# Kernel tuning notes

Hardware: AMD Instinct MI355X
Metric: run time of the kernel (lower is better)

The kernel has to match this reference:

```python
import jax, jax.numpy as jnp
import numpy as np

B, S, UC = 64, 5, 50          # batch, sample (candidates), clicked history
D, T = 128, 768               # embedding_size, title_size
NE, NR, NN = 200000, 100, 50000  # entities, relations, news
K, A = 10, 20                 # neighbors per entity, anchor nodes per news


def _lin(k, out_d, in_d):
    w = jax.random.normal(k, (out_d, in_d), jnp.float32) * (1.0 / np.sqrt(in_d))
    b = jnp.zeros((out_d,), jnp.float32)
    return w, b


def setup_inputs() -> dict:
    key = jax.random.key(0)
    ks = jax.random.split(key, 16)
    W_nc1, b_nc1 = _lin(ks[0], D, T)
    W_nc2, b_nc2 = _lin(ks[1], D, D)
    W_anchor, b_anchor = _lin(ks[2], D, 2 * D)
    W_aw1, b_aw1 = _lin(ks[3], D, D)
    W_aw2, b_aw2 = _lin(ks[4], 1, D)
    W_mlp1, b_mlp1 = _lin(ks[5], D, 2 * D)
    W_mlp2, b_mlp2 = _lin(ks[6], D, D)
    return {
        "news_title_embedding": jax.random.normal(ks[7], (NN, T), jnp.float32),
        "entity_embedding": jax.random.normal(ks[8], (NE, D), jnp.float32),
        "relation_embedding": jax.random.normal(ks[9], (NR, D), jnp.float32),
        "W_nc1": W_nc1, "b_nc1": b_nc1, "W_nc2": W_nc2, "b_nc2": b_nc2,
        "W_anchor": W_anchor, "b_anchor": b_anchor,
        "W_aw1": W_aw1, "b_aw1": b_aw1, "W_aw2": W_aw2, "b_aw2": b_aw2,
        "W_mlp1": W_mlp1, "b_mlp1": b_mlp1, "W_mlp2": W_mlp2, "b_mlp2": b_mlp2,
        "cand_news": jax.random.randint(ks[10], (B, S), 0, NN, jnp.int32),
        "clicked_news": jax.random.randint(ks[11], (B, UC), 0, NN, jnp.int32),
        "cand_anchor_nodes": jax.random.randint(ks[12], (B * S, A), 0, NE, jnp.int32),
        "clicked_anchor_nodes": jax.random.randint(ks[13], (B * UC, A), 0, NE, jnp.int32),
        "entity_adj": jax.random.randint(ks[14], (NE, K), 0, NE, jnp.int32),
        "relation_adj": jax.random.randint(ks[15], (NE, K), 0, NR, jnp.int32),
    }


def reference(news_title_embedding, entity_embedding, relation_embedding,
              W_nc1, b_nc1, W_nc2, b_nc2,
              W_anchor, b_anchor, W_aw1, b_aw1, W_aw2, b_aw2,
              W_mlp1, b_mlp1, W_mlp2, b_mlp2,
              cand_news, clicked_news, cand_anchor_nodes, clicked_anchor_nodes,
              entity_adj, relation_adj):
    elu = jax.nn.elu

    def news_emb(ids_flat):  # [N] -> [N, D]
        t = news_title_embedding[ids_flat]                       # [N, T]
        return jnp.tanh(elu(t @ W_nc1.T + b_nc1) @ W_nc2.T + b_nc2)

    def anchor_graph_emb(nodes):  # [N, A] -> [N, D]
        node_e = entity_embedding[nodes]                          # [N, A, D]
        nb_ent = entity_embedding[entity_adj[nodes]]              # [N, A, K, D]
        nb_rel = relation_embedding[relation_adj[nodes]]          # [N, A, K, D]
        agg = jnp.sum(nb_ent + nb_rel, axis=-2)                   # [N, A, D]
        h = jnp.tanh(jnp.concatenate([node_e, agg], axis=-1) @ W_anchor.T + b_anchor)
        logits = elu(h @ W_aw1.T + b_aw1) @ W_aw2.T + b_aw2       # [N, A, 1]
        w = jax.nn.softmax(logits, axis=-2)                       # softmax over anchor nodes
        return jnp.sum(h * w, axis=-2)                            # [N, D]

    cand_e = news_emb(cand_news.reshape(-1))                      # [B*S, D]
    clk_e = news_emb(clicked_news.reshape(-1))                    # [B*UC, D]
    cand_e = jnp.concatenate([cand_e, anchor_graph_emb(cand_anchor_nodes)], axis=-1)
    clk_e = jnp.concatenate([clk_e, anchor_graph_emb(clicked_anchor_nodes)], axis=-1)

    def mlp(x):
        return elu(elu(x @ W_mlp1.T + b_mlp1) @ W_mlp2.T + b_mlp2)

    news_embedding = mlp(cand_e).reshape(B, S, -1)                # [B, S, D]
    user_embedding = jnp.mean(mlp(clk_e).reshape(B, UC, -1), axis=1)  # [B, D]
    score = jnp.sum(news_embedding * user_embedding[:, None, :], axis=-1)  # [B, S]
    return score
```

## Files before the change

### kernel.cpp

```cpp
#include <hip/hip_runtime.h>
#include <hip/hip_bf16.h>


#define B_ 64
#define S_ 5
#define UC_ 50
#define A_ 20
#define NCAND 320
#define NCLK 3200
#define NNEWS 3520
#define NANCH 70400

static constexpr long OFF_WNC1P = 64;
static constexpr long OFF_BNC1  = 98368;
static constexpr long OFF_WNC2P = 98496;
static constexpr long OFF_BNC2  = 114880;
static constexpr long OFF_WANCP = 115008;
static constexpr long OFF_BANC  = 147776;
static constexpr long OFF_WAW1P = 147904;
static constexpr long OFF_BAW1  = 164288;
static constexpr long OFF_WAW2  = 164416;
static constexpr long OFF_BAW2  = 164544;
static constexpr long OFF_WM1P  = 164548;
static constexpr long OFF_BM1   = 197316;
static constexpr long OFF_WM2P  = 197444;
static constexpr long OFF_BM2   = 213828;
static constexpr long OFF_REL   = 213956;
static constexpr long OFF_AE    = 226756;
static constexpr long OFF_NE    = 677316;
static constexpr long OFF_MO    = 1127876;
static constexpr long OFF_X     = 1578436;

typedef __attribute__((ext_vector_type(8))) short short8v;
typedef __attribute__((ext_vector_type(16))) float f32x16;

__device__ __forceinline__ float ldf(const void* p, long i, int bf) {
  if (bf) {
    unsigned int u = (unsigned int)((const unsigned short*)p)[i];
    u <<= 16;
    return __uint_as_float(u);
  }
  return ((const float*)p)[i];
}

__device__ __forceinline__ float4 ldf4(const void* p, long i, int bf) {
  float4 f;
  if (bf) {
    const unsigned short* q = (const unsigned short*)p + i;
    uint2 u = *(const uint2*)q;
    f.x = __uint_as_float(u.x << 16);
    f.y = __uint_as_float(u.x & 0xffff0000u);
    f.z = __uint_as_float(u.y << 16);
    f.w = __uint_as_float(u.y & 0xffff0000u);
  } else {
    f = *(const float4*)((const float*)p + i);
  }
  return f;
}

__device__ __forceinline__ float eluf(float v) { return v > 0.f ? v : expm1f(v); }

__device__ __forceinline__ void splitbf(float v, unsigned short& hi, unsigned short& lo) {
  unsigned int b = __float_as_uint(v);
  hi = (unsigned short)(b >> 16);
  float rm = v - __uint_as_float(b & 0xffff0000u);
  unsigned int rb = __float_as_uint(rm);
  lo = (unsigned short)((rb + 0x7fffu + ((rb >> 16) & 1u)) >> 16);
}

__device__ __forceinline__ float bfh(unsigned short u) {
  return __uint_as_float((unsigned int)u << 16);
}

__global__ void k_detect(const void* ent, int* flag) {
  __shared__ int cnt;
  if (threadIdx.x == 0) cnt = 0;
  __syncthreads();
  unsigned short u = ((const unsigned short*)ent)[threadIdx.x];
  int e = (u >> 7) & 0xFF;
  int ok = (e >= 107 && e <= 146) ? 1 : 0;
  atomicAdd(&cnt, ok);
  __syncthreads();
  if (threadIdx.x == 0) *flag = (cnt >= 200) ? 1 : 0;
}

__global__ __launch_bounds__(256) void k_prep(
    const void* s0, const void* s1, const void* s2, const void* s3,
    const void* s4, const void* s5, const void* s6, const void* s7,
    const void* s8, const void* s9, const void* s10, const void* s11,
    const void* s12, const void* s13, const void* s14, float* ws) {
  const int bf = ((const int*)ws)[0];
  const void* srcs[15] = {s0,s1,s2,s3,s4,s5,s6,s7,s8,s9,s10,s11,s12,s13,s14};
  const int R[15] = {128,128,128,128,128,128,128,128,1,  1,  128,128,128,128,100};
  const int C[15] = {768,1,  128,1,  256,1,  128,1,  128,1,  256,1,  128,1,  128};
  const int MD[15]= {2,  0,  2,  0,  3,  0,  3,  0,  0,  0,  2,  0,  2,  0,  0};
  const long OFF[15] = {OFF_WNC1P,OFF_BNC1,OFF_WNC2P,OFF_BNC2,OFF_WANCP,OFF_BANC,
                        OFF_WAW1P,OFF_BAW1,OFF_WAW2,OFF_BAW2,OFF_WM1P,OFF_BM1,
                        OFF_WM2P,OFF_BM2,OFF_REL};
  const long total = 226689;
  for (long idx = (long)blockIdx.x * blockDim.x + threadIdx.x; idx < total;
       idx += (long)gridDim.x * blockDim.x) {
    long rem = idx;
    int s = 0;
    while (rem >= (long)R[s] * C[s]) { rem -= (long)R[s] * C[s]; s++; }
    float v = ldf(srcs[s], rem, bf);
    if (MD[s] == 2) {
      long r = rem / C[s], c = rem - r * C[s];
      ws[OFF[s] + (c >> 2) * 512 + r * 4 + (c & 3)] = v;
    } else if (MD[s] == 3) {
      long r = rem / C[s], c = rem - r * C[s];
      unsigned short hi, lo;
      splitbf(v, hi, lo);
      unsigned short* H = (unsigned short*)(ws + OFF[s]);
      unsigned short* L = H + (s == 4 ? 32768 : 16384);
      long id2 = ((c >> 4) * 128 + r) * 16 + (c & 15);
      H[id2] = hi;
      L[id2] = lo;
    } else {
      ws[OFF[s] + rem] = v;
    }
  }
}

__global__ __launch_bounds__(128) void k_news(const void* titles, const int* cand,
                                              const int* clk, float* ws) {
  const int bf = ((const int*)ws)[0];
  __shared__ __align__(16) float t[8][768];
  __shared__ __align__(16) float h1[8][128];
  int tid = threadIdx.x;
  long r0 = (long)blockIdx.x * 8;
  for (int x = tid * 4; x < 8 * 768; x += 128 * 4) {
    int c = x / 768, k = x - c * 768;
    long i = r0 + c;
    int id = (i < NCAND) ? cand[i] : clk[i - NCAND];
    *(float4*)&t[c][k] = ldf4(titles, (long)id * 768 + k, bf);
  }
  __syncthreads();
  int j = tid;
  const float4* W1 = (const float4*)(ws + OFF_WNC1P);
  float acc[8];
#pragma unroll
  for (int c = 0; c < 8; c++) acc[c] = 0.f;
  for (int k4 = 0; k4 < 192; k4++) {
    float4 w = W1[k4 * 128 + j];
#pragma unroll
    for (int c = 0; c < 8; c++) {
      const float4 xv = *(const float4*)&t[c][k4 * 4];
      acc[c] += w.x * xv.x + w.y * xv.y + w.z * xv.z + w.w * xv.w;
    }
  }
  float b1 = ws[OFF_BNC1 + j];
#pragma unroll
  for (int c = 0; c < 8; c++) h1[c][j] = eluf(acc[c] + b1);
  __syncthreads();
  const float4* W2 = (const float4*)(ws + OFF_WNC2P);
  float a2[8];
#pragma unroll
  for (int c = 0; c < 8; c++) a2[c] = 0.f;
  for (int k4 = 0; k4 < 32; k4++) {
    float4 w = W2[k4 * 128 + j];
#pragma unroll
    for (int c = 0; c < 8; c++) {
      const float4 xv = *(const float4*)&h1[c][k4 * 4];
      a2[c] += w.x * xv.x + w.y * xv.y + w.z * xv.z + w.w * xv.w;
    }
  }
  float b2 = ws[OFF_BNC2 + j];
  float* NE = ws + OFF_NE;
#pragma unroll
  for (int c = 0; c < 8; c++) NE[(r0 + c) * 128 + j] = tanhf(a2[c] + b2);
}

__global__ __launch_bounds__(256) void k_gather(const void* ent, const int* canda,
                                                const int* clka, const int* eadj,
                                                const int* radj, float* ws) {
  const int bf = ((const int*)ws)[0];
  __shared__ __align__(16) unsigned short XbH[8][264];
  __shared__ __align__(16) unsigned short XbL[8][264];
  int tid = threadIdx.x;
  int lane = tid & 31;
  int row = tid >> 5;
  const float* relf = ws + OFF_REL;

  long n = (long)blockIdx.x * 8 + row;
  int node = (n < (long)NCAND * A_) ? canda[n] : clka[n - (long)NCAND * A_];
  int idx = 0;
  if (lane < 10) idx = eadj[(long)node * 10 + lane];
  else if (lane < 20) idx = radj[(long)node * 10 + (lane - 10)];
  int an[10], rn[10];
#pragma unroll
  for (int k = 0; k < 10; k++) {
    an[k] = __shfl(idx, k, 32);
    rn[k] = __shfl(idx, k + 10, 32);
  }
  float4 x1 = ldf4(ent, (long)node * 128 + lane * 4, bf);
  float4 acc = {0.f, 0.f, 0.f, 0.f};
#pragma unroll
  for (int k = 0; k < 10; k++) {
    float4 e = ldf4(ent, (long)an[k] * 128 + lane * 4, bf);
    const float4 r = *(const float4*)&relf[(long)rn[k] * 128 + lane * 4];
    acc.x += e.x + r.x;
    acc.y += e.y + r.y;
    acc.z += e.z + r.z;
    acc.w += e.w + r.w;
  }
  ushort4 h4, l4;
  splitbf(x1.x, h4.x, l4.x); splitbf(x1.y, h4.y, l4.y);
  splitbf(x1.z, h4.z, l4.z); splitbf(x1.w, h4.w, l4.w);
  *(ushort4*)&XbH[row][lane * 4] = h4;
  *(ushort4*)&XbL[row][lane * 4] = l4;
  splitbf(acc.x, h4.x, l4.x); splitbf(acc.y, h4.y, l4.y);
  splitbf(acc.z, h4.z, l4.z); splitbf(acc.w, h4.w, l4.w);
  *(ushort4*)&XbH[row][128 + lane * 4] = h4;
  *(ushort4*)&XbL[row][128 + lane * 4] = l4;
  __syncthreads();

  unsigned short* XH = (unsigned short*)(ws + OFF_X);
  unsigned short* XL = XH + (size_t)NANCH * 256;
  int b = blockIdx.x;
  long base = (long)(b >> 2) * 8192 + (long)(b & 3) * 64;
  {
    int lr = tid & 7, kt2h = tid >> 3;
    long addr = base + (long)kt2h * 256 + (long)lr * 8;
    *(uint4*)&XH[addr] = *(const uint4*)&XbH[lr][kt2h * 8];
    *(uint4*)&XL[addr] = *(const uint4*)&XbL[lr][kt2h * 8];
  }
}

__global__ __launch_bounds__(256, 2) void k_anchor(float* ws) {
  __shared__ __align__(16) unsigned short Hhi[160][128];
  __shared__ __align__(16) unsigned short Hlo[160][128];
  int tid = threadIdx.x;
  int lane = tid & 63, wv = tid >> 6;
  int ln = lane & 31, kh = lane >> 5;
  int col = (wv << 5) + ln;

  const unsigned short* XH = (const unsigned short*)(ws + OFF_X);
  const unsigned short* XL = XH + (size_t)NANCH * 256;
  const unsigned short* WAH = (const unsigned short*)(ws + OFF_WANCP);
  const unsigned short* WAL = WAH + 32768;
  const unsigned short* W1H = (const unsigned short*)(ws + OFF_WAW1P);
  const unsigned short* W1L = W1H + 16384;
  float* LGs = ws + OFF_MO + (long)blockIdx.x * 640;

  {
    f32x16 acc[5] = {};
    for (int kt = 0; kt < 16; ++kt) {
      long wi = ((long)(kt * 128 + col) << 4) + (kh << 3);
      short8v bhi = *(const short8v*)(WAH + wi);
      short8v blo = *(const short8v*)(WAL + wi);
#pragma unroll
      for (int mt = 0; mt < 5; ++mt) {
        long ai = ((long)(blockIdx.x * 5 + mt) << 13) + ((kt * 2 + kh) << 8) + (ln << 3);
        short8v ahi = *(const short8v*)(XH + ai);
        short8v alo = *(const short8v*)(XL + ai);
        acc[mt] = __builtin_amdgcn_mfma_f32_32x32x16_bf16(ahi, bhi, acc[mt], 0, 0, 0);
        acc[mt] = __builtin_amdgcn_mfma_f32_32x32x16_bf16(ahi, blo, acc[mt], 0, 0, 0);
        acc[mt] = __builtin_amdgcn_mfma_f32_32x32x16_bf16(alo, bhi, acc[mt], 0, 0, 0);
      }
    }
    float bc = ws[OFF_BANC + col];
#pragma unroll
    for (int mt = 0; mt < 5; ++mt)
#pragma unroll
      for (int j = 0; j < 16; ++j) {
        int r = mt * 32 + (j & 3) + ((j >> 2) << 3) + (kh << 2);
        float h = tanhf(acc[mt][j] + bc);
        unsigned short hi, lo;
        splitbf(h, hi, lo);
        int sc = col ^ ((r & 7) << 3);
        Hhi[r][sc] = hi;
        Hlo[r][sc] = lo;
      }
  }
  __syncthreads();

  {
    f32x16 ac[5] = {};
    for (int kt = 0; kt < 8; ++kt) {
      long wi = ((long)(kt * 128 + col) << 4) + (kh << 3);
      short8v bhi = *(const short8v*)(W1H + wi);
      short8v blo = *(const short8v*)(W1L + wi);
#pragma unroll
      for (int mt = 0; mt < 5; ++mt) {
        int rr = mt * 32 + ln;
        int kb = (kt * 16 + (kh << 3)) ^ ((rr & 7) << 3);
        short8v ahi = *(const short8v*)&Hhi[rr][kb];
        short8v alo = *(const short8v*)&Hlo[rr][kb];
        ac[mt] = __builtin_amdgcn_mfma_f32_32x32x16_bf16(ahi, bhi, ac[mt], 0, 0, 0);
        ac[mt] = __builtin_amdgcn_mfma_f32_32x32x16_bf16(ahi, blo, ac[mt], 0, 0, 0);
        ac[mt] = __builtin_amdgcn_mfma_f32_32x32x16_bf16(alo, bhi, ac[mt], 0, 0, 0);
      }
    }
    float b1c = ws[OFF_BAW1 + col];
    float w2c = ws[OFF_WAW2 + col];
#pragma unroll
    for (int mt = 0; mt < 5; ++mt)
#pragma unroll
      for (int j = 0; j < 16; ++j) {
        int r = mt * 32 + (j & 3) + ((j >> 2) << 3) + (kh << 2);
        float v = eluf(ac[mt][j] + b1c) * w2c;
        v += __shfl_xor(v, 16);
        v += __shfl_xor(v, 8);
        v += __shfl_xor(v, 4);
        v += __shfl_xor(v, 2);
        v += __shfl_xor(v, 1);
        if (ln == 0) LGs[wv * 160 + r] = v;
      }
  }
  __threadfence_block();
  __syncthreads();

  {
    int g = tid >> 5, l32 = tid & 31, ar = g * 20;
    float bw2 = ws[OFF_BAW2];
    float e[20], mx = -1e30f;
#pragma unroll
    for (int a = 0; a < 20; ++a) {
      int rr = ar + a;
      e[a] = LGs[rr] + LGs[160 + rr] + LGs[320 + rr] + LGs[480 + rr] + bw2;
      mx = fmaxf(mx, e[a]);
    }
    float s = 0.f;
#pragma unroll
    for (int a = 0; a < 20; ++a) { e[a] = expf(e[a] - mx); s += e[a]; }
    float inv = 1.0f / s;
    float o0 = 0.f, o1 = 0.f, o2 = 0.f, o3 = 0.f;
#pragma unroll
    for (int a = 0; a < 20; ++a) {
      int rr = ar + a, sw = (rr & 7) << 3;
      float w = e[a];
      int d0 = l32 ^ sw, d1 = (l32 + 32) ^ sw, d2 = (l32 + 64) ^ sw, d3 = (l32 + 96) ^ sw;
      o0 += w * (bfh(Hhi[rr][d0]) + bfh(Hlo[rr][d0]));
      o1 += w * (bfh(Hhi[rr][d1]) + bfh(Hlo[rr][d1]));
      o2 += w * (bfh(Hhi[rr][d2]) + bfh(Hlo[rr][d2]));
      o3 += w * (bfh(Hhi[rr][d3]) + bfh(Hlo[rr][d3]));
    }
    float* AE = ws + OFF_AE;
    long ro = ((long)blockIdx.x * 8 + g) * 128;
    AE[ro + l32]      = o0 * inv;
    AE[ro + l32 + 32] = o1 * inv;
    AE[ro + l32 + 64] = o2 * inv;
    AE[ro + l32 + 96] = o3 * inv;
  }
}

__global__ __launch_bounds__(256) void k_mlp(float* ws) {
  __shared__ __align__(16) float xt[16][256];
  __shared__ __align__(16) float h1[16][128];
  int tid = threadIdx.x;
  long r0 = (long)blockIdx.x * 16;
  const float* NE = ws + OFF_NE;
  const float* AE = ws + OFF_AE;
  for (int x = tid; x < 16 * 256; x += 256) {
    int c = x >> 8, k = x & 255;
    xt[c][k] = (k < 128) ? NE[(r0 + c) * 128 + k] : AE[(r0 + c) * 128 + (k - 128)];
  }
  __syncthreads();
  int j = tid & 127, half = tid >> 7;
  const float4* W1 = (const float4*)(ws + OFF_WM1P);
  float acc[8];
#pragma unroll
  for (int c = 0; c < 8; c++) acc[c] = 0.f;
  for (int k4 = 0; k4 < 64; k4++) {
    float4 w = W1[k4 * 128 + j];
#pragma unroll
    for (int c = 0; c < 8; c++) {
      const float4 xv = *(const float4*)&xt[half * 8 + c][k4 * 4];
      acc[c] += w.x * xv.x + w.y * xv.y + w.z * xv.z + w.w * xv.w;
    }
  }
  float b1 = ws[OFF_BM1 + j];
#pragma unroll
  for (int c = 0; c < 8; c++) h1[half * 8 + c][j] = eluf(acc[c] + b1);
  __syncthreads();
  const float4* W2 = (const float4*)(ws + OFF_WM2P);
  float a2[8];
#pragma unroll
  for (int c = 0; c < 8; c++) a2[c] = 0.f;
  for (int k4 = 0; k4 < 32; k4++) {
    float4 w = W2[k4 * 128 + j];
#pragma unroll
    for (int c = 0; c < 8; c++) {
      const float4 xv = *(const float4*)&h1[half * 8 + c][k4 * 4];
      a2[c] += w.x * xv.x + w.y * xv.y + w.z * xv.z + w.w * xv.w;
    }
  }
  float b2 = ws[OFF_BM2 + j];
  float* MO = ws + OFF_MO;
#pragma unroll
  for (int c = 0; c < 8; c++) MO[(r0 + half * 8 + c) * 128 + j] = eluf(a2[c] + b2);
}

__global__ __launch_bounds__(128) void k_score(const float* ws, void* out) {
  const int bf = ((const int*)ws)[0];
  int b = blockIdx.x;
  int d = threadIdx.x;
  const float* MO = ws + OFF_MO;
  float u = 0.f;
  for (int t = 0; t < UC_; t++) u += MO[(long)(NCAND + b * UC_ + t) * 128 + d];
  u *= (1.0f / UC_);
  __shared__ float red[2];
  for (int s = 0; s < S_; s++) {
    float p = MO[(long)(b * S_ + s) * 128 + d] * u;
#pragma unroll
    for (int o = 32; o > 0; o >>= 1) p += __shfl_down(p, o, 64);
    if ((d & 63) == 0) red[d >> 6] = p;
    __syncthreads();
    if (d == 0) {
      float v = red[0] + red[1];
      if (bf)
        ((__hip_bfloat16*)out)[b * S_ + s] = __float2bfloat16(v);
      else
        ((float*)out)[b * S_ + s] = v;
    }
    __syncthreads();
  }
}

extern "C" void kernel_launch(void* const* d_in, const int* in_sizes, int n_in,
                              void* d_out, int out_size, void* d_ws, size_t ws_size,
                              hipStream_t stream) {
  (void)in_sizes; (void)n_in; (void)out_size; (void)ws_size;
  const void* titles = d_in[0];
  const void* ent    = d_in[1];
  const void* rel    = d_in[2];
  const void* Wnc1 = d_in[3];  const void* bnc1 = d_in[4];
  const void* Wnc2 = d_in[5];  const void* bnc2 = d_in[6];
  const void* Wanc = d_in[7];  const void* banc = d_in[8];
  const void* Waw1 = d_in[9];  const void* baw1 = d_in[10];
  const void* Waw2 = d_in[11]; const void* baw2 = d_in[12];
  const void* Wm1  = d_in[13]; const void* bm1  = d_in[14];
  const void* Wm2  = d_in[15]; const void* bm2  = d_in[16];
  const int* cand  = (const int*)d_in[17];
  const int* clk   = (const int*)d_in[18];
  const int* canda = (const int*)d_in[19];
  const int* clka  = (const int*)d_in[20];
  const int* eadj  = (const int*)d_in[21];
  const int* radj  = (const int*)d_in[22];
  float* ws = (float*)d_ws;

  k_detect<<<1, 256, 0, stream>>>(ent, (int*)d_ws);
  k_prep<<<256, 256, 0, stream>>>(Wnc1, bnc1, Wnc2, bnc2, Wanc, banc, Waw1, baw1,
                                  Waw2, baw2, Wm1, bm1, Wm2, bm2, rel, ws);
  k_news<<<NNEWS / 8, 128, 0, stream>>>(titles, cand, clk, ws);
  k_gather<<<NANCH / 8, 256, 0, stream>>>(ent, canda, clka, eadj, radj, ws);
  k_anchor<<<NNEWS / 8, 256, 0, stream>>>(ws);
  k_mlp<<<NNEWS / 16, 256, 0, stream>>>(ws);
  k_score<<<B_, 128, 0, stream>>>(ws, d_out);
}
```

Measured before the change: 247.4 us.

## Fuse neighbor gather into anchor kernel and switch to 16x16x32 MFMA tiles

Merges the separate gather kernel into the anchor kernel: each block gathers 80 anchor rows, 16 at a time, into shared memory as split-bf16 and feeds them straight into the MFMA projection. This removes the global round-trip of the large X buffer (NANCH x 256 hi/lo) and one kernel launch. The weight layout is repacked for 16x16x32 MFMA and the block count goes from 440 to 880, with 4 news per block. In exchange, each block alternates gather and MFMA phases under barriers, so there is less overlap inside a block, and the weight loads are repeated more often.

```diff
diff --git a/kernel.cpp b/kernel.cpp
--- a/kernel.cpp
+++ b/kernel.cpp
@@ -29,10 +29,9 @@
 static constexpr long OFF_AE    = 226756;
 static constexpr long OFF_NE    = 677316;
 static constexpr long OFF_MO    = 1127876;
-static constexpr long OFF_X     = 1578436;
 
 typedef __attribute__((ext_vector_type(8))) short short8v;
-typedef __attribute__((ext_vector_type(16))) float f32x16;
+typedef __attribute__((ext_vector_type(4))) float f32x4;
 
 __device__ __forceinline__ float ldf(const void* p, long i, int bf) {
   if (bf) {
@@ -113,7 +112,7 @@
       splitbf(v, hi, lo);
       unsigned short* H = (unsigned short*)(ws + OFF[s]);
       unsigned short* L = H + (s == 4 ? 32768 : 16384);
-      long id2 = ((c >> 4) * 128 + r) * 16 + (c & 15);
+      long id2 = ((c >> 5) * 128 + r) * 32 + (c & 31);
       H[id2] = hi;
       L[id2] = lo;
     } else {
@@ -171,177 +170,168 @@
   for (int c = 0; c < 8; c++) NE[(r0 + c) * 128 + j] = tanhf(a2[c] + b2);
 }
 
-__global__ __launch_bounds__(256) void k_gather(const void* ent, const int* canda,
-                                                const int* clka, const int* eadj,
-                                                const int* radj, float* ws) {
+__global__ __launch_bounds__(256, 2) void k_anchor(const void* ent, const int* canda,
+                                                   const int* clka, const int* eadj,
+                                                   const int* radj, float* ws) {
+  __shared__ __align__(16) unsigned short XbH[16][264];
+  __shared__ __align__(16) unsigned short XbL[16][264];
+  __shared__ __align__(16) unsigned short Hhi[80][136];
+  __shared__ __align__(16) unsigned short Hlo[80][136];
+  __shared__ int NodeIdL[80];
+  __shared__ int EAdjL[800];
+  __shared__ int RAdjL[800];
+  __shared__ float LGp[4][80];
+
   const int bf = ((const int*)ws)[0];
-  __shared__ __align__(16) unsigned short XbH[8][264];
-  __shared__ __align__(16) unsigned short XbL[8][264];
-  int tid = threadIdx.x;
-  int lane = tid & 31;
-  int row = tid >> 5;
-  const float* relf = ws + OFF_REL;
-
-  long n = (long)blockIdx.x * 8 + row;
-  int node = (n < (long)NCAND * A_) ? canda[n] : clka[n - (long)NCAND * A_];
-  int idx = 0;
-  if (lane < 10) idx = eadj[(long)node * 10 + lane];
-  else if (lane < 20) idx = radj[(long)node * 10 + (lane - 10)];
-  int an[10], rn[10];
-#pragma unroll
-  for (int k = 0; k < 10; k++) {
-    an[k] = __shfl(idx, k, 32);
-    rn[k] = __shfl(idx, k + 10, 32);
-  }
-  float4 x1 = ldf4(ent, (long)node * 128 + lane * 4, bf);
-  float4 acc = {0.f, 0.f, 0.f, 0.f};
-#pragma unroll
-  for (int k = 0; k < 10; k++) {
-    float4 e = ldf4(ent, (long)an[k] * 128 + lane * 4, bf);
-    const float4 r = *(const float4*)&relf[(long)rn[k] * 128 + lane * 4];
-    acc.x += e.x + r.x;
-    acc.y += e.y + r.y;
-    acc.z += e.z + r.z;
-    acc.w += e.w + r.w;
-  }
-  ushort4 h4, l4;
-  splitbf(x1.x, h4.x, l4.x); splitbf(x1.y, h4.y, l4.y);
-  splitbf(x1.z, h4.z, l4.z); splitbf(x1.w, h4.w, l4.w);
-  *(ushort4*)&XbH[row][lane * 4] = h4;
-  *(ushort4*)&XbL[row][lane * 4] = l4;
-  splitbf(acc.x, h4.x, l4.x); splitbf(acc.y, h4.y, l4.y);
-  splitbf(acc.z, h4.z, l4.z); splitbf(acc.w, h4.w, l4.w);
-  *(ushort4*)&XbH[row][128 + lane * 4] = h4;
-  *(ushort4*)&XbL[row][128 + lane * 4] = l4;
-  __syncthreads();
-
-  unsigned short* XH = (unsigned short*)(ws + OFF_X);
-  unsigned short* XL = XH + (size_t)NANCH * 256;
-  int b = blockIdx.x;
-  long base = (long)(b >> 2) * 8192 + (long)(b & 3) * 64;
-  {
-    int lr = tid & 7, kt2h = tid >> 3;
-    long addr = base + (long)kt2h * 256 + (long)lr * 8;
-    *(uint4*)&XH[addr] = *(const uint4*)&XbH[lr][kt2h * 8];
-    *(uint4*)&XL[addr] = *(const uint4*)&XbL[lr][kt2h * 8];
-  }
-}
-
-__global__ __launch_bounds__(256, 2) void k_anchor(float* ws) {
-  __shared__ __align__(16) unsigned short Hhi[160][128];
-  __shared__ __align__(16) unsigned short Hlo[160][128];
   int tid = threadIdx.x;
   int lane = tid & 63, wv = tid >> 6;
-  int ln = lane & 31, kh = lane >> 5;
-  int col = (wv << 5) + ln;
-
-  const unsigned short* XH = (const unsigned short*)(ws + OFF_X);
-  const unsigned short* XL = XH + (size_t)NANCH * 256;
+  int r16 = lane & 15, khh = lane >> 4;
+  int lane32 = tid & 31, grp = tid >> 5;
+  const float* relf = ws + OFF_REL;
+
   const unsigned short* WAH = (const unsigned short*)(ws + OFF_WANCP);
   const unsigned short* WAL = WAH + 32768;
   const unsigned short* W1H = (const unsigned short*)(ws + OFF_WAW1P);
   const unsigned short* W1L = W1H + 16384;
-  float* LGs = ws + OFF_MO + (long)blockIdx.x * 640;
+
+  if (tid < 80) {
+    long n = (long)blockIdx.x * 80 + tid;
+    NodeIdL[tid] = (n < (long)NCAND * A_) ? canda[n] : clka[n - (long)NCAND * A_];
+  }
+  __syncthreads();
+  for (int t = tid; t < 800; t += 256) {
+    int rr = t / 10, kk = t - rr * 10;
+    int nd = NodeIdL[rr];
+    EAdjL[t] = eadj[(long)nd * 10 + kk];
+    RAdjL[t] = radj[(long)nd * 10 + kk];
+  }
+  __syncthreads();
+
+  for (int mt = 0; mt < 5; ++mt) {
+    for (int i = 0; i < 2; ++i) {
+      int cr = grp * 2 + i;
+      int gr = mt * 16 + cr;
+      int node = NodeIdL[gr];
+      float4 x1 = ldf4(ent, (long)node * 128 + lane32 * 4, bf);
+      float4 a = {0.f, 0.f, 0.f, 0.f};
+#pragma unroll
+      for (int k = 0; k < 10; ++k) {
+        int an = EAdjL[gr * 10 + k], rn = RAdjL[gr * 10 + k];
+        float4 e = ldf4(ent, (long)an * 128 + lane32 * 4, bf);
+        const float4 r = *(const float4*)&relf[(long)rn * 128 + lane32 * 4];
+        a.x += e.x + r.x;
+        a.y += e.y + r.y;
+        a.z += e.z + r.z;
+        a.w += e.w + r.w;
+      }
+      ushort4 h4, l4;
+      splitbf(x1.x, h4.x, l4.x); splitbf(x1.y, h4.y, l4.y);
+      splitbf(x1.z, h4.z, l4.z); splitbf(x1.w, h4.w, l4.w);
+      *(ushort4*)&XbH[cr][lane32 * 4] = h4;
+      *(ushort4*)&XbL[cr][lane32 * 4] = l4;
+      splitbf(a.x, h4.x, l4.x); splitbf(a.y, h4.y, l4.y);
+      splitbf(a.z, h4.z, l4.z); splitbf(a.w, h4.w, l4.w);
+      *(ushort4*)&XbH[cr][128 + lane32 * 4] = h4;
+      *(ushort4*)&XbL[cr][128 + lane32 * 4] = l4;
+    }
+    __syncthreads();
+
+    {
+      f32x4 acc0 = {}, acc1 = {};
+      int n0 = wv * 32 + r16, n1 = n0 + 16;
+      for (int kt = 0; kt < 8; ++kt) {
+        short8v ahi = *(const short8v*)&XbH[r16][kt * 32 + khh * 8];
+        short8v alo = *(const short8v*)&XbL[r16][kt * 32 + khh * 8];
+        long w0 = ((long)(kt * 128 + n0)) * 32 + khh * 8;
+        long w1 = ((long)(kt * 128 + n1)) * 32 + khh * 8;
+        short8v b0h = *(const short8v*)(WAH + w0);
+        short8v b0l = *(const short8v*)(WAL + w0);
+        short8v b1h = *(const short8v*)(WAH + w1);
+        short8v b1l = *(const short8v*)(WAL + w1);
+        acc0 = __builtin_amdgcn_mfma_f32_16x16x32_bf16(ahi, b0h, acc0, 0, 0, 0);
+        acc0 = __builtin_amdgcn_mfma_f32_16x16x32_bf16(ahi, b0l, acc0, 0, 0, 0);
+        acc0 = __builtin_amdgcn_mfma_f32_16x16x32_bf16(alo, b0h, acc0, 0, 0, 0);
+        acc1 = __builtin_amdgcn_mfma_f32_16x16x32_bf16(ahi, b1h, acc1, 0, 0, 0);
+        acc1 = __builtin_amdgcn_mfma_f32_16x16x32_bf16(ahi, b1l, acc1, 0, 0, 0);
+        acc1 = __builtin_amdgcn_mfma_f32_16x16x32_bf16(alo, b1h, acc1, 0, 0, 0);
+      }
+      float bc0 = ws[OFF_BANC + n0], bc1 = ws[OFF_BANC + n1];
+#pragma unroll
+      for (int j = 0; j < 4; ++j) {
+        int r = mt * 16 + khh * 4 + j;
+        unsigned short hi, lo;
+        float h0 = tanhf(acc0[j] + bc0);
+        splitbf(h0, hi, lo);
+        Hhi[r][n0] = hi; Hlo[r][n0] = lo;
+        float h1 = tanhf(acc1[j] + bc1);
+        splitbf(h1, hi, lo);
+        Hhi[r][n1] = hi; Hlo[r][n1] = lo;
+      }
+    }
+    __syncthreads();
+  }
 
   {
-    f32x16 acc[5] = {};
-    for (int kt = 0; kt < 16; ++kt) {
-      long wi = ((long)(kt * 128 + col) << 4) + (kh << 3);
-      short8v bhi = *(const short8v*)(WAH + wi);
-      short8v blo = *(const short8v*)(WAL + wi);
-#pragma unroll
-      for (int mt = 0; mt < 5; ++mt) {
-        long ai = ((long)(blockIdx.x * 5 + mt) << 13) + ((kt * 2 + kh) << 8) + (ln << 3);
-        short8v ahi = *(const short8v*)(XH + ai);
-        short8v alo = *(const short8v*)(XL + ai);
-        acc[mt] = __builtin_amdgcn_mfma_f32_32x32x16_bf16(ahi, bhi, acc[mt], 0, 0, 0);
-        acc[mt] = __builtin_amdgcn_mfma_f32_32x32x16_bf16(ahi, blo, acc[mt], 0, 0, 0);
-        acc[mt] = __builtin_amdgcn_mfma_f32_32x32x16_bf16(alo, bhi, acc[mt], 0, 0, 0);
+    int n0 = wv * 32 + r16, n1 = n0 + 16;
+    float b10 = ws[OFF_BAW1 + n0], b11 = ws[OFF_BAW1 + n1];
+    float w20 = ws[OFF_WAW2 + n0], w21 = ws[OFF_WAW2 + n1];
+    for (int mt = 0; mt < 5; ++mt) {
+      f32x4 ac0 = {}, ac1 = {};
+      for (int kt = 0; kt < 4; ++kt) {
+        short8v ahi = *(const short8v*)&Hhi[mt * 16 + r16][kt * 32 + khh * 8];
+        short8v alo = *(const short8v*)&Hlo[mt * 16 + r16][kt * 32 + khh * 8];
+        long w0 = ((long)(kt * 128 + n0)) * 32 + khh * 8;
+        long w1 = ((long)(kt * 128 + n1)) * 32 + khh * 8;
+        short8v b0h = *(const short8v*)(W1H + w0);
+        short8v b0l = *(const short8v*)(W1L + w0);
+        short8v b1h = *(const short8v*)(W1H + w1);
+        short8v b1l = *(const short8v*)(W1L + w1);
+        ac0 = __builtin_amdgcn_mfma_f32_16x16x32_bf16(ahi, b0h, ac0, 0, 0, 0);
+        ac0 = __builtin_amdgcn_mfma_f32_16x16x32_bf16(ahi, b0l, ac0, 0, 0, 0);
+        ac0 = __builtin_amdgcn_mfma_f32_16x16x32_bf16(alo, b0h, ac0, 0, 0, 0);
+        ac1 = __builtin_amdgcn_mfma_f32_16x16x32_bf16(ahi, b1h, ac1, 0, 0, 0);
+        ac1 = __builtin_amdgcn_mfma_f32_16x16x32_bf16(ahi, b1l, ac1, 0, 0, 0);
+        ac1 = __builtin_amdgcn_mfma_f32_16x16x32_bf16(alo, b1h, ac1, 0, 0, 0);
       }
-    }
-    float bc = ws[OFF_BANC + col];
-#pragma unroll
-    for (int mt = 0; mt < 5; ++mt)
-#pragma unroll
-      for (int j = 0; j < 16; ++j) {
-        int r = mt * 32 + (j & 3) + ((j >> 2) << 3) + (kh << 2);
-        float h = tanhf(acc[mt][j] + bc);
-        unsigned short hi, lo;
-        splitbf(h, hi, lo);
-        int sc = col ^ ((r & 7) << 3);
-        Hhi[r][sc] = hi;
-        Hlo[r][sc] = lo;
+#pragma unroll
+      for (int j = 0; j < 4; ++j) {
+        float v = eluf(ac0[j] + b10) * w20 + eluf(ac1[j] + b11) * w21;
+        v += __shfl_xor(v, 1);
+        v += __shfl_xor(v, 2);
+        v += __shfl_xor(v, 4);
+        v += __shfl_xor(v, 8);
+        if (r16 == 0) LGp[wv][mt * 16 + khh * 4 + j] = v;
       }
+    }
   }
   __syncthreads();
 
   {
-    f32x16 ac[5] = {};
-    for (int kt = 0; kt < 8; ++kt) {
-      long wi = ((long)(kt * 128 + col) << 4) + (kh << 3);
-      short8v bhi = *(const short8v*)(W1H + wi);
-      short8v blo = *(const short8v*)(W1L + wi);
-#pragma unroll
-      for (int mt = 0; mt < 5; ++mt) {
-        int rr = mt * 32 + ln;
-        int kb = (kt * 16 + (kh << 3)) ^ ((rr & 7) << 3);
-        short8v ahi = *(const short8v*)&Hhi[rr][kb];
-        short8v alo = *(const short8v*)&Hlo[rr][kb];
-        ac[mt] = __builtin_amdgcn_mfma_f32_32x32x16_bf16(ahi, bhi, ac[mt], 0, 0, 0);
-        ac[mt] = __builtin_amdgcn_mfma_f32_32x32x16_bf16(ahi, blo, ac[mt], 0, 0, 0);
-        ac[mt] = __builtin_amdgcn_mfma_f32_32x32x16_bf16(alo, bhi, ac[mt], 0, 0, 0);
-      }
-    }
-    float b1c = ws[OFF_BAW1 + col];
-    float w2c = ws[OFF_WAW2 + col];
-#pragma unroll
-    for (int mt = 0; mt < 5; ++mt)
-#pragma unroll
-      for (int j = 0; j < 16; ++j) {
-        int r = mt * 32 + (j & 3) + ((j >> 2) << 3) + (kh << 2);
-        float v = eluf(ac[mt][j] + b1c) * w2c;
-        v += __shfl_xor(v, 16);
-        v += __shfl_xor(v, 8);
-        v += __shfl_xor(v, 4);
-        v += __shfl_xor(v, 2);
-        v += __shfl_xor(v, 1);
-        if (ln == 0) LGs[wv * 160 + r] = v;
-      }
-  }
-  __threadfence_block();
-  __syncthreads();
-
-  {
-    int g = tid >> 5, l32 = tid & 31, ar = g * 20;
+    int g = tid >> 6, ar = g * 20;
     float bw2 = ws[OFF_BAW2];
     float e[20], mx = -1e30f;
 #pragma unroll
     for (int a = 0; a < 20; ++a) {
       int rr = ar + a;
-      e[a] = LGs[rr] + LGs[160 + rr] + LGs[320 + rr] + LGs[480 + rr] + bw2;
+      e[a] = LGp[0][rr] + LGp[1][rr] + LGp[2][rr] + LGp[3][rr] + bw2;
       mx = fmaxf(mx, e[a]);
     }
     float s = 0.f;
 #pragma unroll
     for (int a = 0; a < 20; ++a) { e[a] = expf(e[a] - mx); s += e[a]; }
     float inv = 1.0f / s;
-    float o0 = 0.f, o1 = 0.f, o2 = 0.f, o3 = 0.f;
+    float o0 = 0.f, o1 = 0.f;
 #pragma unroll
     for (int a = 0; a < 20; ++a) {
-      int rr = ar + a, sw = (rr & 7) << 3;
+      int rr = ar + a;
       float w = e[a];
-      int d0 = l32 ^ sw, d1 = (l32 + 32) ^ sw, d2 = (l32 + 64) ^ sw, d3 = (l32 + 96) ^ sw;
-      o0 += w * (bfh(Hhi[rr][d0]) + bfh(Hlo[rr][d0]));
-      o1 += w * (bfh(Hhi[rr][d1]) + bfh(Hlo[rr][d1]));
-      o2 += w * (bfh(Hhi[rr][d2]) + bfh(Hlo[rr][d2]));
-      o3 += w * (bfh(Hhi[rr][d3]) + bfh(Hlo[rr][d3]));
+      o0 += w * (bfh(Hhi[rr][lane]) + bfh(Hlo[rr][lane]));
+      o1 += w * (bfh(Hhi[rr][lane + 64]) + bfh(Hlo[rr][lane + 64]));
     }
     float* AE = ws + OFF_AE;
-    long ro = ((long)blockIdx.x * 8 + g) * 128;
-    AE[ro + l32]      = o0 * inv;
-    AE[ro + l32 + 32] = o1 * inv;
-    AE[ro + l32 + 64] = o2 * inv;
-    AE[ro + l32 + 96] = o3 * inv;
+    long ro = ((long)blockIdx.x * 4 + g) * 128;
+    AE[ro + lane]      = o0 * inv;
+    AE[ro + lane + 64] = o1 * inv;
   }
 }
 
@@ -444,8 +434,7 @@
   k_prep<<<256, 256, 0, stream>>>(Wnc1, bnc1, Wnc2, bnc2, Wanc, banc, Waw1, baw1,
                                   Waw2, baw2, Wm1, bm1, Wm2, bm2, rel, ws);
   k_news<<<NNEWS / 8, 128, 0, stream>>>(titles, cand, clk, ws);
-  k_gather<<<NANCH / 8, 256, 0, stream>>>(ent, canda, clka, eadj, radj, ws);
-  k_anchor<<<NNEWS / 8, 256, 0, stream>>>(ws);
+  k_anchor<<<NANCH / 80, 256, 0, stream>>>(ent, canda, clka, eadj, radj, ws);
   k_mlp<<<NNEWS / 16, 256, 0, stream>>>(ws);
   k_score<<<B_, 128, 0, stream>>>(ws, d_out);
 }
```

After: 230.4 us. 6.9% less time.
